# Kernel tuning notes

Hardware: AMD Instinct MI355X
Metric: run time of the kernel (lower is better)

Reference implementation:

```python
import jax, jax.numpy as jnp
import numpy as np

N, V, E_PER = 8, 4608, 73728          # batch, nodes per graph, edges per graph
D_IN, C, NCLS = 1, 512, 3             # node feat dim, embed dim, classes
E = N * E_PER
LN_EPS = 1e-5


def setup_inputs() -> dict:
    key = jax.random.key(0)
    ks = jax.random.split(key, 12)
    x = jax.random.normal(ks[0], (N, 1, V, D_IN), jnp.float32)
    edge_index = jax.random.randint(ks[1], (2, E), 0, V, dtype=jnp.int32)
    edge_weight = jax.random.uniform(ks[2], (E,), jnp.float32)
    # GCNConv params: layer0 maps D_IN->C, layers 1..2 map C->C (weight [in,out], bias [out])
    w0 = jax.random.normal(ks[3], (D_IN, C), jnp.float32) * 0.02
    b0 = jnp.zeros((C,), jnp.float32)
    w1 = jax.random.normal(ks[4], (C, C), jnp.float32) * 0.02
    b1 = jnp.zeros((C,), jnp.float32)
    w2 = jax.random.normal(ks[5], (C, C), jnp.float32) * 0.02
    b2 = jnp.zeros((C,), jnp.float32)
    ln_g = jnp.ones((C,), jnp.float32)
    ln_b = jnp.zeros((C,), jnp.float32)
    head_w = jax.random.normal(ks[6], (C, NCLS), jnp.float32) * 2e-5
    head_b = jnp.log(jnp.full((NCLS,), 1.0 / NCLS, jnp.float32))
    return {"x": x, "edge_weight": edge_weight, "w0": w0, "b0": b0,
            "w1": w1, "b1": b1, "w2": w2, "b2": b2,
            "ln_g": ln_g, "ln_b": ln_b, "head_w": head_w, "head_b": head_b,
            "edge_index": edge_index}


def layer_norm(h, g, b):
    mu = h.mean(-1, keepdims=True)
    var = ((h - mu) ** 2).mean(-1, keepdims=True)
    return (h - mu) * jax.lax.rsqrt(var + LN_EPS) * g + b


def reference(x, edge_weight, w0, b0, w1, b1, w2, b2, ln_g, ln_b, head_w, head_b, edge_index):
    n, t, v, d = x.shape
    nv = n * v
    h = x.reshape(nv, d)
    # batch-offset local edge indices (edges are contiguous per graph)
    offs = jnp.repeat(jnp.arange(n, dtype=edge_index.dtype) * v, edge_index.shape[1] // n)
    src = edge_index[0] + offs
    tgt = edge_index[1] + offs
    # GCN norm with self-loops (fill weight 1.0), symmetric deg^-1/2 normalization
    loop = jnp.arange(nv, dtype=src.dtype)
    src_f = jnp.concatenate([src, loop])
    tgt_f = jnp.concatenate([tgt, loop])
    ew_f = jnp.concatenate([edge_weight, jnp.ones((nv,), edge_weight.dtype)])
    deg = jax.ops.segment_sum(ew_f, tgt_f, num_segments=nv)
    deg_safe = jnp.where(deg > 0, deg, 1.0)
    dinv = jnp.where(deg > 0, jax.lax.rsqrt(deg_safe), 0.0)
    norm = dinv[src_f] * ew_f * dinv[tgt_f]
    for w, bb in ((w0, b0), (w1, b1), (w2, b2)):
        hw = h @ w                                   # [NV, C]
        msg = norm[:, None] * hw[src_f]              # gather + scale  [E+NV, C]
        h = jax.ops.segment_sum(msg, tgt_f, num_segments=nv) + bb
        h = jax.nn.relu(h)
        h = layer_norm(h, ln_g, ln_b)
        # dropout is identity in eval mode
    pooled = h.reshape(n, v, -1).max(axis=1)         # global_max_pool (contiguous batch)
    pooled = layer_norm(pooled, ln_g, ln_b)
    return pooled @ head_w + head_b                  # [N, NCLS]
```

## Files before the change

### kernel.cpp

```cpp
#include <hip/hip_runtime.h>
#include <hip/hip_bf16.h>
#include <stdint.h>

#define N_GRAPH 8
#define V_NODES 4608
#define E_PER   73728
#define NV      (N_GRAPH * V_NODES)
#define E_TOT   (N_GRAPH * E_PER)
#define C       512
#define NCLS    3
#define LN_EPS  1e-5f
#define POOL_CHUNKS 36
#define SCAN_BLOCKS 144
#define DPB     576

typedef __attribute__((ext_vector_type(8))) short short8;
typedef __attribute__((ext_vector_type(4))) float floatx4;
typedef __attribute__((address_space(1))) void v_g;
typedef __attribute__((address_space(3))) void v_l;


__device__ inline float waveReduceSum(float v) {
#pragma unroll
    for (int o = 32; o > 0; o >>= 1) v += __shfl_down(v, o, 64);
    return v;
}

__device__ inline float waveAllSum(float v) {
#pragma unroll
    for (int o = 32; o > 0; o >>= 1) v += __shfl_xor(v, o, 64);
    return v;
}

__device__ inline float blockSum512(float v, volatile float* sred) {
    float s = waveReduceSum(v);
    if ((threadIdx.x & 63) == 0) sred[threadIdx.x >> 6] = s;
    __syncthreads();
    float t = 0.f;
#pragma unroll
    for (int i = 0; i < 8; i++) t += sred[i];
    __syncthreads();
    return t;
}

__device__ inline unsigned short f2bf(float f) {
    uint32_t u = __float_as_uint(f);
    u += 0x7fffu + ((u >> 16) & 1u);
    return (unsigned short)(u >> 16);
}
__device__ inline float bf2f(unsigned short b) {
    return __uint_as_float(((uint32_t)b) << 16);
}


__launch_bounds__(1024)
__global__ void k_deg_lds(const int* __restrict__ ei, const float* __restrict__ ew,
                          float* __restrict__ dinv, int* __restrict__ counts) {
    __shared__ float degl[DPB];
    __shared__ int   cntl[DPB];
    const int b = blockIdx.x;
    const int g = b >> 3, part = b & 7;
    const int t0 = part * DPB;
    const int tid = threadIdx.x;
    for (int i = tid; i < DPB; i += 1024) { degl[i] = 1.0f; cntl[i] = 0; }
    __syncthreads();
    const int*   tgt = ei + E_TOT + g * E_PER;
    const float* w   = ew + g * E_PER;
    for (int e = tid; e < E_PER; e += 1024) {
        int tl = tgt[e] - t0;
        if ((unsigned)tl < DPB) {
            atomicAdd(&degl[tl], w[e]);
            atomicAdd(&cntl[tl], 1);
        }
    }
    __syncthreads();
    for (int i = tid; i < DPB; i += 1024) {
        int node = g * V_NODES + t0 + i;
        dinv[node]   = rsqrtf(degl[i]);
        counts[node] = cntl[i];
    }
}


__global__ void k_scan1(const int* __restrict__ counts, int* __restrict__ row_ptr,
                        int* __restrict__ bsum) {
    __shared__ int sh[256];
    const int b = blockIdx.x, tid = threadIdx.x;
    const int idx = b * 256 + tid;
    int v = counts[idx];
    sh[tid] = v;
    __syncthreads();
#pragma unroll
    for (int off = 1; off < 256; off <<= 1) {
        int t = (tid >= off) ? sh[tid - off] : 0;
        __syncthreads();
        sh[tid] += t;
        __syncthreads();
    }
    row_ptr[idx] = sh[tid] - v;
    if (tid == 255) bsum[b] = sh[255];
}

__global__ void k_scan2(int* __restrict__ bsum) {
    __shared__ int sh[256];
    const int tid = threadIdx.x;
    int v = (tid < SCAN_BLOCKS) ? bsum[tid] : 0;
    sh[tid] = v;
    __syncthreads();
#pragma unroll
    for (int off = 1; off < 256; off <<= 1) {
        int t = (tid >= off) ? sh[tid - off] : 0;
        __syncthreads();
        sh[tid] += t;
        __syncthreads();
    }
    if (tid < SCAN_BLOCKS) bsum[tid] = sh[tid] - v;
}

__global__ void k_scan3(int* __restrict__ row_ptr, const int* __restrict__ bsum) {
    const int b = blockIdx.x, tid = threadIdx.x;
    const int idx = b * 256 + tid;
    row_ptr[idx] += bsum[b];
    if (idx == 0) row_ptr[NV] = E_TOT;
}

__launch_bounds__(1024)
__global__ void k_fill_lds(const int* __restrict__ ei, const float* __restrict__ ew,
                           const float* __restrict__ dinv, const int* __restrict__ row_ptr,
                           int* __restrict__ col_idx, float* __restrict__ val) {
    __shared__ int curl[DPB];
    const int b = blockIdx.x;
    const int g = b >> 3, part = b & 7;
    const int t0 = part * DPB;
    const int nbase = g * V_NODES + t0;
    const int tid = threadIdx.x;
    for (int i = tid; i < DPB; i += 1024) curl[i] = row_ptr[nbase + i];
    __syncthreads();
    const int*   src = ei + g * E_PER;
    const int*   tgt = ei + E_TOT + g * E_PER;
    const float* w   = ew + g * E_PER;
    for (int e = tid; e < E_PER; e += 1024) {
        int tl = tgt[e] - t0;
        if ((unsigned)tl < DPB) {
            int s = src[e] + g * V_NODES;
            int pos = atomicAdd(&curl[tl], 1);
            col_idx[pos] = s;
            val[pos] = dinv[s] * w[e] * dinv[nbase + tl];
        }
    }
}


__global__ void k_wt(const float* __restrict__ w1, const float* __restrict__ w2,
                     unsigned short* __restrict__ wt1, unsigned short* __restrict__ wt2) {
    int idx = blockIdx.x * 256 + threadIdx.x;
    int which = idx >> 18;
    int rem = idx & 0x3ffff;
    int n = rem >> 9, k = rem & 511;
    const float* W = which ? w2 : w1;
    unsigned short* WT = which ? wt2 : wt1;
    WT[n * C + k] = f2bf(W[k * C + n]);
}


__global__ void k_agg0_scalar(const float* __restrict__ x, const int* __restrict__ row_ptr,
                              const int* __restrict__ col_idx, const float* __restrict__ val,
                              const float* __restrict__ dinv, float* __restrict__ s0) {
    int t = blockIdx.x * 256 + threadIdx.x;
    if (t >= NV) return;
    float dt = dinv[t];
    float acc = dt * dt * x[t];
    int e1 = row_ptr[t + 1];
    for (int e = row_ptr[t]; e < e1; e++)
        acc += val[e] * x[col_idx[e]];
    s0[t] = acc;
}

__launch_bounds__(128)
__global__ void k_l0post(const float* __restrict__ s0, const float* __restrict__ w0,
                         const float* __restrict__ b0, const float* __restrict__ ln_g,
                         const float* __restrict__ ln_b, unsigned short* __restrict__ out) {
    const int t = blockIdx.x;
    const int tid = threadIdx.x;
    const int c4 = tid << 2;
    float s = s0[t];
    float4 w = *reinterpret_cast<const float4*>(&w0[c4]);
    float4 bb = *reinterpret_cast<const float4*>(&b0[c4]);
    float vx = fmaxf(s * w.x + bb.x, 0.f);
    float vy = fmaxf(s * w.y + bb.y, 0.f);
    float vz = fmaxf(s * w.z + bb.z, 0.f);
    float vw = fmaxf(s * w.w + bb.w, 0.f);
    __shared__ float redA[2], redB[2];
    float wsum = waveReduceSum(vx + vy + vz + vw);
    if ((tid & 63) == 0) redA[tid >> 6] = wsum;
    __syncthreads();
    float mu = (redA[0] + redA[1]) * (1.0f / C);
    float dx = vx - mu, dy = vy - mu, dz = vz - mu, dw = vw - mu;
    float wsq = waveReduceSum(dx * dx + dy * dy + dz * dz + dw * dw);
    if ((tid & 63) == 0) redB[tid >> 6] = wsq;
    __syncthreads();
    float rstd = rsqrtf((redB[0] + redB[1]) * (1.0f / C) + LN_EPS);
    float4 g = *reinterpret_cast<const float4*>(&ln_g[c4]);
    float4 b = *reinterpret_cast<const float4*>(&ln_b[c4]);
    ushort4 o = { f2bf(dx * rstd * g.x + b.x), f2bf(dy * rstd * g.y + b.y),
                  f2bf(dz * rstd * g.z + b.z), f2bf(dw * rstd * g.w + b.w) };
    reinterpret_cast<ushort4*>(out)[(size_t)t * 128 + tid] = o;
}


__launch_bounds__(256)
__global__ void k_gemm_mfma(const unsigned short* __restrict__ A,
                            const unsigned short* __restrict__ WT,
                            unsigned short* __restrict__ Bout) {
    __shared__ short8 lA[512];
    __shared__ short8 lB[512];
    const int tid = threadIdx.x;
    const int lane = tid & 63;
    const int wave = tid >> 6;
    const int wr = wave >> 1, wc = wave & 1;
    const int l15 = lane & 15, kg = lane >> 4;
    const int m0 = blockIdx.x * 128;
    const int n0 = blockIdx.y * 128;

    floatx4 acc[4][4] = {};

    const int s0i = tid, s1i = 256 + tid;
    const int kgs0 = s0i >> 7, idx0 = s0i & 127;
    const int kgs1 = s1i >> 7, idx1 = s1i & 127;
    const unsigned short* gA0 = A + (size_t)(m0 + idx0) * C + kgs0 * 8;
    const unsigned short* gA1 = A + (size_t)(m0 + idx1) * C + kgs1 * 8;
    const unsigned short* gB0 = WT + (size_t)(n0 + idx0) * C + kgs0 * 8;
    const unsigned short* gB1 = WT + (size_t)(n0 + idx1) * C + kgs1 * 8;

    for (int k0 = 0; k0 < C; k0 += 32) {
        __builtin_amdgcn_global_load_lds((v_g*)(gA0 + k0), (v_l*)&lA[s0i], 16, 0, 0);
        __builtin_amdgcn_global_load_lds((v_g*)(gA1 + k0), (v_l*)&lA[s1i], 16, 0, 0);
        __builtin_amdgcn_global_load_lds((v_g*)(gB0 + k0), (v_l*)&lB[s0i], 16, 0, 0);
        __builtin_amdgcn_global_load_lds((v_g*)(gB1 + k0), (v_l*)&lB[s1i], 16, 0, 0);
        asm volatile("s_waitcnt vmcnt(0)" ::: "memory");
        __syncthreads();

        short8 af[4], bf[4];
#pragma unroll
        for (int mi = 0; mi < 4; mi++)
            af[mi] = lA[kg * 128 + wr * 64 + mi * 16 + l15];
#pragma unroll
        for (int ni = 0; ni < 4; ni++)
            bf[ni] = lB[kg * 128 + wc * 64 + ni * 16 + l15];
#pragma unroll
        for (int mi = 0; mi < 4; mi++)
#pragma unroll
            for (int ni = 0; ni < 4; ni++)
                acc[mi][ni] = __builtin_amdgcn_mfma_f32_16x16x32_bf16(
                    af[mi], bf[ni], acc[mi][ni], 0, 0, 0);
        __syncthreads();
    }

#pragma unroll
    for (int mi = 0; mi < 4; mi++) {
#pragma unroll
        for (int ni = 0; ni < 4; ni++) {
            int n = n0 + wc * 64 + ni * 16 + l15;
#pragma unroll
            for (int r = 0; r < 4; r++) {
                int m = m0 + wr * 64 + mi * 16 + kg * 4 + r;
                Bout[(size_t)m * C + n] = f2bf(acc[mi][ni][r]);
            }
        }
    }
}


__launch_bounds__(256)
__global__ void k_agg(const unsigned short* __restrict__ hw, const int* __restrict__ row_ptr,
                      const int* __restrict__ col_idx, const float* __restrict__ val,
                      const float* __restrict__ dinv, const float* __restrict__ bias,
                      const float* __restrict__ ln_g, const float* __restrict__ ln_b,
                      unsigned short* __restrict__ out) {
    const int b = blockIdx.x;
    const int wv = threadIdx.x >> 6;
    const int lane = threadIdx.x & 63;
    const int t = (b & 7) * V_NODES + ((b >> 3) << 2) + wv;
    const int e0 = row_ptr[t], e1 = row_ptr[t + 1];
    const short8* hw8 = reinterpret_cast<const short8*>(hw);

    const float dt = dinv[t];
    const float selfw = dt * dt;
    short8 hs = hw8[(size_t)t * 64 + lane];
    float a[8];
#pragma unroll
    for (int i = 0; i < 8; i++) a[i] = selfw * bf2f((unsigned short)hs[i]);

    int e = e0;
    for (; e + 4 <= e1; e += 4) {
        int i0 = col_idx[e], i1 = col_idx[e + 1], i2 = col_idx[e + 2], i3 = col_idx[e + 3];
        float w0 = val[e], w1 = val[e + 1], w2 = val[e + 2], w3 = val[e + 3];
        short8 h0 = hw8[(size_t)i0 * 64 + lane];
        short8 h1 = hw8[(size_t)i1 * 64 + lane];
        short8 h2 = hw8[(size_t)i2 * 64 + lane];
        short8 h3 = hw8[(size_t)i3 * 64 + lane];
#pragma unroll
        for (int i = 0; i < 8; i++) a[i] += w0 * bf2f((unsigned short)h0[i]);
#pragma unroll
        for (int i = 0; i < 8; i++) a[i] += w1 * bf2f((unsigned short)h1[i]);
#pragma unroll
        for (int i = 0; i < 8; i++) a[i] += w2 * bf2f((unsigned short)h2[i]);
#pragma unroll
        for (int i = 0; i < 8; i++) a[i] += w3 * bf2f((unsigned short)h3[i]);
    }
    for (; e < e1; e++) {
        int is = col_idx[e];
        float w = val[e];
        short8 hv = hw8[(size_t)is * 64 + lane];
#pragma unroll
        for (int i = 0; i < 8; i++) a[i] += w * bf2f((unsigned short)hv[i]);
    }

    const int c8 = lane << 3;
    float4 bb0 = *reinterpret_cast<const float4*>(&bias[c8]);
    float4 bb1 = *reinterpret_cast<const float4*>(&bias[c8 + 4]);
    a[0] = fmaxf(a[0] + bb0.x, 0.f); a[1] = fmaxf(a[1] + bb0.y, 0.f);
    a[2] = fmaxf(a[2] + bb0.z, 0.f); a[3] = fmaxf(a[3] + bb0.w, 0.f);
    a[4] = fmaxf(a[4] + bb1.x, 0.f); a[5] = fmaxf(a[5] + bb1.y, 0.f);
    a[6] = fmaxf(a[6] + bb1.z, 0.f); a[7] = fmaxf(a[7] + bb1.w, 0.f);

    float s = a[0] + a[1] + a[2] + a[3] + a[4] + a[5] + a[6] + a[7];
    float mu = waveAllSum(s) * (1.0f / C);
    float sq = 0.f;
#pragma unroll
    for (int i = 0; i < 8; i++) { float d = a[i] - mu; sq += d * d; }
    float rstd = rsqrtf(waveAllSum(sq) * (1.0f / C) + LN_EPS);

    float4 g0 = *reinterpret_cast<const float4*>(&ln_g[c8]);
    float4 g1 = *reinterpret_cast<const float4*>(&ln_g[c8 + 4]);
    float4 z0 = *reinterpret_cast<const float4*>(&ln_b[c8]);
    float4 z1 = *reinterpret_cast<const float4*>(&ln_b[c8 + 4]);
    short8 o;
    o[0] = (short)f2bf((a[0] - mu) * rstd * g0.x + z0.x);
    o[1] = (short)f2bf((a[1] - mu) * rstd * g0.y + z0.y);
    o[2] = (short)f2bf((a[2] - mu) * rstd * g0.z + z0.z);
    o[3] = (short)f2bf((a[3] - mu) * rstd * g0.w + z0.w);
    o[4] = (short)f2bf((a[4] - mu) * rstd * g1.x + z1.x);
    o[5] = (short)f2bf((a[5] - mu) * rstd * g1.y + z1.y);
    o[6] = (short)f2bf((a[6] - mu) * rstd * g1.z + z1.z);
    o[7] = (short)f2bf((a[7] - mu) * rstd * g1.w + z1.w);
    reinterpret_cast<short8*>(out)[(size_t)t * 64 + lane] = o;
}


__global__ void k_pool1(const unsigned short* __restrict__ h, float* __restrict__ pmax) {
    int g = blockIdx.x, chunk = blockIdx.y;
    int c = threadIdx.x;
    int r0 = g * V_NODES + chunk * 128;
    float m = -1e30f;
#pragma unroll 4
    for (int r = 0; r < 128; r++)
        m = fmaxf(m, bf2f(h[(size_t)(r0 + r) * C + c]));
    pmax[((size_t)g * POOL_CHUNKS + chunk) * C + c] = m;
}

__global__ void k_pool2_head(const float* __restrict__ pmax, const float* __restrict__ ln_g,
                             const float* __restrict__ ln_b, const float* __restrict__ hw,
                             const float* __restrict__ hb, float* __restrict__ out) {
    __shared__ float sred[8];
    int g = blockIdx.x;
    int c = threadIdx.x;
    float m = -1e30f;
#pragma unroll
    for (int j = 0; j < POOL_CHUNKS; j++)
        m = fmaxf(m, pmax[((size_t)g * POOL_CHUNKS + j) * C + c]);
    float total = blockSum512(m, sred);
    float mu = total * (1.0f / C);
    float d = m - mu;
    float var = blockSum512(d * d, sred) * (1.0f / C);
    float rstd = rsqrtf(var + LN_EPS);
    float p = d * rstd * ln_g[c] + ln_b[c];
    float r0 = blockSum512(p * hw[c * NCLS + 0], sred);
    float r1 = blockSum512(p * hw[c * NCLS + 1], sred);
    float r2 = blockSum512(p * hw[c * NCLS + 2], sred);
    if (threadIdx.x == 0) {
        out[g * NCLS + 0] = r0 + hb[0];
        out[g * NCLS + 1] = r1 + hb[1];
        out[g * NCLS + 2] = r2 + hb[2];
    }
}


extern "C" void kernel_launch(void* const* d_in, const int* in_sizes, int n_in,
                              void* d_out, int out_size, void* d_ws, size_t ws_size,
                              hipStream_t stream) {
    const float* x      = (const float*)d_in[0];
    const float* ew     = (const float*)d_in[1];
    const float* w0     = (const float*)d_in[2];
    const float* b0     = (const float*)d_in[3];
    const float* w1     = (const float*)d_in[4];
    const float* b1     = (const float*)d_in[5];
    const float* w2     = (const float*)d_in[6];
    const float* b2     = (const float*)d_in[7];
    const float* ln_g   = (const float*)d_in[8];
    const float* ln_b   = (const float*)d_in[9];
    const float* head_w = (const float*)d_in[10];
    const float* head_b = (const float*)d_in[11];
    const int*   ei     = (const int*)d_in[12];
    float* out = (float*)d_out;

    char* p = (char*)d_ws;
    auto alloc = [&](size_t bytes) { void* r = p; p += (bytes + 255) & ~255ull; return r; };
    unsigned short* bufA = (unsigned short*)alloc((size_t)NV * C * 2);
    unsigned short* bufB = (unsigned short*)alloc((size_t)NV * C * 2);
    unsigned short* wt1  = (unsigned short*)alloc((size_t)C * C * 2);
    unsigned short* wt2  = (unsigned short*)alloc((size_t)C * C * 2);
    float* s0      = (float*)alloc((size_t)NV * 4);
    float* dinv    = (float*)alloc((size_t)NV * 4);
    int*   counts  = (int*)alloc((size_t)NV * 4);
    int*   row_ptr = (int*)alloc((size_t)(NV + 1) * 4);
    int*   bsum    = (int*)alloc((size_t)SCAN_BLOCKS * 4);
    int*   col_idx = (int*)alloc((size_t)E_TOT * 4);
    float* val     = (float*)alloc((size_t)E_TOT * 4);
    float* pmax    = (float*)alloc((size_t)N_GRAPH * POOL_CHUNKS * C * 4);

    k_deg_lds<<<64, 1024, 0, stream>>>(ei, ew, dinv, counts);
    k_scan1<<<SCAN_BLOCKS, 256, 0, stream>>>(counts, row_ptr, bsum);
    k_scan2<<<1, 256, 0, stream>>>(bsum);
    k_scan3<<<SCAN_BLOCKS, 256, 0, stream>>>(row_ptr, bsum);
    k_fill_lds<<<64, 1024, 0, stream>>>(ei, ew, dinv, row_ptr, col_idx, val);
    k_wt<<<(2 * C * C) / 256, 256, 0, stream>>>(w1, w2, wt1, wt2);

    k_agg0_scalar<<<NV / 256, 256, 0, stream>>>(x, row_ptr, col_idx, val, dinv, s0);
    k_l0post<<<NV, 128, 0, stream>>>(s0, w0, b0, ln_g, ln_b, bufA);

    k_gemm_mfma<<<dim3(NV / 128, C / 128), 256, 0, stream>>>(bufA, wt1, bufB);
    k_agg<<<NV / 4, 256, 0, stream>>>(bufB, row_ptr, col_idx, val, dinv, b1, ln_g, ln_b, bufA);

    k_gemm_mfma<<<dim3(NV / 128, C / 128), 256, 0, stream>>>(bufA, wt2, bufB);
    k_agg<<<NV / 4, 256, 0, stream>>>(bufB, row_ptr, col_idx, val, dinv, b2, ln_g, ln_b, bufA);

    k_pool1<<<dim3(N_GRAPH, POOL_CHUNKS), C, 0, stream>>>(bufA, pmax);
    k_pool2_head<<<N_GRAPH, C, 0, stream>>>(pmax, ln_g, ln_b, head_w, head_b, out);
}
```

Measured before the change: 452.6 us.

## Build CSR via per-edge-chunk LDS histograms instead of per-target-range scans

```diff
diff --git a/kernel.cpp b/kernel.cpp
--- a/kernel.cpp
+++ b/kernel.cpp
@@ -12,7 +12,8 @@
 #define LN_EPS  1e-5f
 #define POOL_CHUNKS 36
 #define SCAN_BLOCKS 144
-#define DPB     576
+#define SUBB    32
+#define EPSB    (E_PER / SUBB)
 
 typedef __attribute__((ext_vector_type(8))) short short8;
 typedef __attribute__((ext_vector_type(4))) float floatx4;
@@ -53,32 +54,49 @@
 }
 
 
-__launch_bounds__(1024)
-__global__ void k_deg_lds(const int* __restrict__ ei, const float* __restrict__ ew,
-                          float* __restrict__ dinv, int* __restrict__ counts) {
-    __shared__ float degl[DPB];
-    __shared__ int   cntl[DPB];
-    const int b = blockIdx.x;
-    const int g = b >> 3, part = b & 7;
-    const int t0 = part * DPB;
+__launch_bounds__(256)
+__global__ void k_hist(const int* __restrict__ ei, const float* __restrict__ ew,
+                       int* __restrict__ hist_c, float* __restrict__ hist_d) {
+    __shared__ int   lcnt[V_NODES];
+    __shared__ float ldeg[V_NODES];
+    const int g = blockIdx.x >> 5, j = blockIdx.x & 31;
     const int tid = threadIdx.x;
-    for (int i = tid; i < DPB; i += 1024) { degl[i] = 1.0f; cntl[i] = 0; }
-    __syncthreads();
-    const int*   tgt = ei + E_TOT + g * E_PER;
-    const float* w   = ew + g * E_PER;
-    for (int e = tid; e < E_PER; e += 1024) {
-        int tl = tgt[e] - t0;
-        if ((unsigned)tl < DPB) {
-            atomicAdd(&degl[tl], w[e]);
-            atomicAdd(&cntl[tl], 1);
-        }
-    }
-    __syncthreads();
-    for (int i = tid; i < DPB; i += 1024) {
-        int node = g * V_NODES + t0 + i;
-        dinv[node]   = rsqrtf(degl[i]);
-        counts[node] = cntl[i];
-    }
+    for (int i = tid; i < V_NODES; i += 256) { lcnt[i] = 0; ldeg[i] = 0.f; }
+    __syncthreads();
+    const int ebase = g * E_PER + j * EPSB;
+    const int*   tgt = ei + E_TOT + ebase;
+    const float* w   = ew + ebase;
+    for (int i = tid; i < EPSB; i += 256) {
+        int t = tgt[i];
+        atomicAdd(&lcnt[t], 1);
+        atomicAdd(&ldeg[t], w[i]);
+    }
+    __syncthreads();
+    const size_t hb = ((size_t)g * SUBB + j) * V_NODES;
+    for (int i = tid; i < V_NODES; i += 256) {
+        hist_c[hb + i] = lcnt[i];
+        hist_d[hb + i] = ldeg[i];
+    }
+}
+
+__global__ void k_reduce(int* __restrict__ hist_c, const float* __restrict__ hist_d,
+                         int* __restrict__ counts, float* __restrict__ dinv) {
+    const int node = blockIdx.x * 256 + threadIdx.x;
+    if (node >= NV) return;
+    const int g = node / V_NODES, t = node - g * V_NODES;
+    const size_t base = (size_t)g * SUBB * V_NODES + t;
+    int c = 0;
+    float d = 1.0f;
+#pragma unroll 8
+    for (int j = 0; j < SUBB; j++) {
+        const size_t idx = base + (size_t)j * V_NODES;
+        int cc = hist_c[idx];
+        hist_c[idx] = c;
+        c += cc;
+        d += hist_d[idx];
+    }
+    counts[node] = c;
+    dinv[node] = rsqrtf(d);
 }
 
 
@@ -124,29 +142,29 @@
     if (idx == 0) row_ptr[NV] = E_TOT;
 }
 
-__launch_bounds__(1024)
-__global__ void k_fill_lds(const int* __restrict__ ei, const float* __restrict__ ew,
-                           const float* __restrict__ dinv, const int* __restrict__ row_ptr,
-                           int* __restrict__ col_idx, float* __restrict__ val) {
-    __shared__ int curl[DPB];
-    const int b = blockIdx.x;
-    const int g = b >> 3, part = b & 7;
-    const int t0 = part * DPB;
-    const int nbase = g * V_NODES + t0;
+__launch_bounds__(256)
+__global__ void k_fill2(const int* __restrict__ ei, const float* __restrict__ ew,
+                        const float* __restrict__ dinv, const int* __restrict__ row_ptr,
+                        const int* __restrict__ hist_c,
+                        int* __restrict__ col_idx, float* __restrict__ val) {
+    __shared__ int cur[V_NODES];
+    const int g = blockIdx.x >> 5, j = blockIdx.x & 31;
     const int tid = threadIdx.x;
-    for (int i = tid; i < DPB; i += 1024) curl[i] = row_ptr[nbase + i];
-    __syncthreads();
-    const int*   src = ei + g * E_PER;
-    const int*   tgt = ei + E_TOT + g * E_PER;
-    const float* w   = ew + g * E_PER;
-    for (int e = tid; e < E_PER; e += 1024) {
-        int tl = tgt[e] - t0;
-        if ((unsigned)tl < DPB) {
-            int s = src[e] + g * V_NODES;
-            int pos = atomicAdd(&curl[tl], 1);
-            col_idx[pos] = s;
-            val[pos] = dinv[s] * w[e] * dinv[nbase + tl];
-        }
+    const int gV = g * V_NODES;
+    const size_t hb = ((size_t)g * SUBB + j) * V_NODES;
+    for (int i = tid; i < V_NODES; i += 256)
+        cur[i] = row_ptr[gV + i] + hist_c[hb + i];
+    __syncthreads();
+    const int ebase = g * E_PER + j * EPSB;
+    const int*   src = ei + ebase;
+    const int*   tgt = ei + E_TOT + ebase;
+    const float* w   = ew + ebase;
+    for (int i = tid; i < EPSB; i += 256) {
+        int t = tgt[i];
+        int s = src[i] + gV;
+        int pos = atomicAdd(&cur[t], 1);
+        col_idx[pos] = s;
+        val[pos] = dinv[s] * w[i] * dinv[gV + t];
     }
 }
 
@@ -415,15 +433,18 @@
     int*   counts  = (int*)alloc((size_t)NV * 4);
     int*   row_ptr = (int*)alloc((size_t)(NV + 1) * 4);
     int*   bsum    = (int*)alloc((size_t)SCAN_BLOCKS * 4);
+    int*   hist_c  = (int*)alloc((size_t)N_GRAPH * SUBB * V_NODES * 4);
+    float* hist_d  = (float*)alloc((size_t)N_GRAPH * SUBB * V_NODES * 4);
     int*   col_idx = (int*)alloc((size_t)E_TOT * 4);
     float* val     = (float*)alloc((size_t)E_TOT * 4);
     float* pmax    = (float*)alloc((size_t)N_GRAPH * POOL_CHUNKS * C * 4);
 
-    k_deg_lds<<<64, 1024, 0, stream>>>(ei, ew, dinv, counts);
+    k_hist<<<N_GRAPH * SUBB, 256, 0, stream>>>(ei, ew, hist_c, hist_d);
+    k_reduce<<<SCAN_BLOCKS, 256, 0, stream>>>(hist_c, hist_d, counts, dinv);
     k_scan1<<<SCAN_BLOCKS, 256, 0, stream>>>(counts, row_ptr, bsum);
     k_scan2<<<1, 256, 0, stream>>>(bsum);
     k_scan3<<<SCAN_BLOCKS, 256, 0, stream>>>(row_ptr, bsum);
-    k_fill_lds<<<64, 1024, 0, stream>>>(ei, ew, dinv, row_ptr, col_idx, val);
+    k_fill2<<<N_GRAPH * SUBB, 256, 0, stream>>>(ei, ew, dinv, row_ptr, hist_c, col_idx, val);
     k_wt<<<(2 * C * C) / 256, 256, 0, stream>>>(w1, w2, wt1, wt2);
 
     k_agg0_scalar<<<NV / 256, 256, 0, stream>>>(x, row_ptr, col_idx, val, dinv, s0);
```

After: 375.7 us. -17.0%, faster.
